# Optimization experiments

Measured on AMD Instinct MI355X. Metric: run time of the kernel, lower is better.

Reference implementation:

```python
import jax, jax.numpy as jnp
import numpy as np

ABS_DIM, HIDDEN, ACTION_DIM, N_TASKS, B = 512, 512, 18, 16, 8192
W_SCALE = 0.001


def setup_inputs() -> dict:
    key = jax.random.key(0)
    k1, k2, k3, k4, k5 = jax.random.split(key, 5)
    x = jax.random.normal(k1, (B, ABS_DIM), dtype=jnp.float32)
    task_id = jax.random.randint(k2, (B,), 0, N_TASKS)
    action = jax.random.randint(k3, (B,), 0, ACTION_DIM)
    # Per-task weight banks (MultiLinear), w_scale=0.001
    W1 = jax.random.normal(k4, (N_TASKS, ABS_DIM, HIDDEN), dtype=jnp.float32) * W_SCALE
    b1 = jnp.zeros((N_TASKS, HIDDEN), dtype=jnp.float32)
    W2 = jax.random.normal(k5, (N_TASKS, HIDDEN, ACTION_DIM), dtype=jnp.float32) * W_SCALE
    b2 = jnp.zeros((N_TASKS, ACTION_DIM), dtype=jnp.float32)
    return {"x": x, "task_id": task_id, "action": action,
            "W1": W1, "b1": b1, "W2": W2, "b2": b2}


def _multi_linear(x, W, b, task_id):
    # x: [B, din], W: [T, din, dout], b: [T, dout]
    # Compute all experts then select per-sample (dense grouped-GEMM form).
    y_all = jnp.einsum('bi,tio->tbo', x, W) + b[:, None, :]  # [T, B, dout]
    rows = jnp.arange(x.shape[0])
    return y_all[task_id, rows]  # [B, dout]


def reference(x, task_id, action, W1, b1, W2, b2):
    h = jax.nn.relu(_multi_linear(x, W1, b1, task_id))          # [B, H]
    logits = _multi_linear(h, W2, b2, task_id)                  # [B, A]
    logprobs = jax.nn.log_softmax(logits, axis=1)               # [B, A]
    rows = jnp.arange(x.shape[0])
    log_pi_a = logprobs[rows, action][:, None]                  # [B, 1]
    ent = -jnp.sum(jnp.exp(logprobs) * logprobs, axis=1, keepdims=True)  # [B, 1]
    # forward output: concat of log_pi_a and entropy (action passes through)
    return jnp.concatenate([log_pi_a, ent], axis=1)             # [B, 2]
```

## Files before the change

kernel.cpp:

```cpp
#include <hip/hip_runtime.h>
#include <hip/hip_bf16.h>

#define B_N   8192
#define DIN   512
#define DH    512
#define NACT  18
#define NTASK 16
#define BM    64
#define BN    64
#define BK    32
#define PJ    20
#define NSLOT 1280
#define SPILL 256

typedef __attribute__((ext_vector_type(8))) short  short8v;
typedef __attribute__((ext_vector_type(8))) unsigned short ushort8v;
typedef __attribute__((ext_vector_type(4))) unsigned short ushort4v;
typedef __attribute__((ext_vector_type(4))) float  float4v;
typedef __attribute__((ext_vector_type(2))) float  float2v;

typedef const __attribute__((address_space(1))) void* gas_ptr;
typedef __attribute__((address_space(3))) void* las_ptr;

__device__ __forceinline__ unsigned short f2bf(float f) {
  union { float f; unsigned int u; } c; c.f = f;
  unsigned int u = c.u;
  u += 0x7fffu + ((u >> 16) & 1u);
  return (unsigned short)(u >> 16);
}

__global__ __launch_bounds__(256) void k_prep(
    const float* __restrict__ W1, const float* __restrict__ W2,
    const int* __restrict__ task_id,
    short* __restrict__ W1T, short* __restrict__ W2T,
    int* __restrict__ tbl, int* __restrict__ rowidx) {
  __shared__ __align__(16) char ldsT[64 * 144];
  __shared__ float ldsB[64 * 19];
  __shared__ int c4[4][NTASK], cur4[4][NTASK];
  int bx = blockIdx.x, tid = threadIdx.x;

  if (bx == 0) {
    if (tid < 64) ((int*)c4)[tid] = 0;
    __syncthreads();
    for (int i = tid; i < B_N; i += 256)
      atomicAdd(&c4[i >> 11][task_id[i]], 1);
    __syncthreads();
    if (tid == 0) {
      int acc = 0;
#pragma unroll
      for (int t = 0; t < NTASK; ++t) {
        int c = c4[0][t] + c4[1][t] + c4[2][t] + c4[3][t];
        tbl[t] = c; tbl[16 + t] = acc;
        int o = acc;
#pragma unroll
        for (int q = 0; q < 4; ++q) { cur4[q][t] = o; o += c4[q][t]; }
        acc += c;
      }
    }
    __syncthreads();
    for (int i = tid; i < B_N; i += 256) {
      int t = task_id[i];
      rowidx[atomicAdd(&cur4[i >> 11][t], 1)] = i;
    }
  } else if (bx <= 1024) {
    int r = bx & 7;
    int q = ((bx - r) >> 3) - (r == 0 ? 1 : 0);
    int t = r + ((q >> 6) << 3);
    int sub = q & 63;
    int kb = sub >> 3, nb = sub & 7;
    int nc4 = tid & 15, kr4 = tid >> 4;
    const float* src = W1 + ((size_t)t * DIN + (size_t)(kb * 64 + kr4 * 4)) * DH
                          + nb * 64 + nc4 * 4;
    float4v r0 = *(const float4v*)(src);
    float4v r1 = *(const float4v*)(src + DH);
    float4v r2 = *(const float4v*)(src + 2 * DH);
    float4v r3 = *(const float4v*)(src + 3 * DH);
#pragma unroll
    for (int i = 0; i < 4; ++i) {
      int n = nc4 * 4 + i;
      ushort4v pk;
      pk[0] = f2bf(r0[i]); pk[1] = f2bf(r1[i]);
      pk[2] = f2bf(r2[i]); pk[3] = f2bf(r3[i]);
      int c = (kr4 >> 1) ^ ((n >> 2) & 7);
      *(ushort4v*)(ldsT + n * 144 + c * 16 + (kr4 & 1) * 8) = pk;
    }
    __syncthreads();
    int n = tid >> 2, k16 = (tid & 3) << 4;
    int c0 = k16 >> 3;
    int f  = (n >> 2) & 7;
    ushort8v v0 = *(ushort8v*)(ldsT + n * 144 + ((c0 ^ f) * 16));
    ushort8v v1 = *(ushort8v*)(ldsT + n * 144 + (((c0 + 1) ^ f) * 16));
    short* dst = W1T + ((size_t)t * DH + nb * 64 + n) * DIN + kb * 64 + k16;
    *(ushort8v*)dst       = v0;
    *(ushort8v*)(dst + 8) = v1;
  } else {
    int u = bx - 1025;
    int t = u >> 3, k0 = (u & 7) * 64;
    for (int i = tid; i < 64 * NACT; i += 256) {
      int kk = i / NACT, j = i - kk * NACT;
      ldsB[kk * 19 + j] = W2[((size_t)t * DIN + k0 + kk) * NACT + j];
    }
    __syncthreads();
    for (int o = tid; o < 32 * 64; o += 256) {
      int j = o >> 6, kk = o & 63;
      float val = (j < NACT) ? ldsB[kk * 19 + j] : 0.0f;
      W2T[((size_t)t * 32 + j) * DIN + k0 + kk] = (short)f2bf(val);
    }
  }
}

__global__ __launch_bounds__(256, 5) void k_gemm1(
    const float* __restrict__ x, const float* __restrict__ bias1,
    const short* __restrict__ W1T, const short* __restrict__ W2Tg,
    const int* __restrict__ tbl, const int* __restrict__ rowidx,
    float* __restrict__ pbuf) {
  __shared__ __align__(16) short sA[2][BM * 40];
  __shared__ __align__(16) short sB[2][BN * BK];
  short* sH  = sA[0];
  short* sW2 = sB[0];
  __shared__ int s_rows[64];
  int tid = threadIdx.x, lane = tid & 63, wave = tid >> 6;

  int b = blockIdx.x;
  int t = -1, rel = 0;
  if (b < NSLOT) {
    int r = b & 7, q = b >> 3;
    int n0t = (tbl[r] + 63) >> 6, n1t = (tbl[r + 8] + 63) >> 6;
    if (q < 8 * n0t) { t = r; rel = q; }
    else if (q < 8 * (n0t + n1t)) { t = r + 8; rel = q - 8 * n0t; }
    else return;
  } else {
    int j = b - NSLOT;
    for (int r = 0; r < 8; ++r) {
      int n0t = (tbl[r] + 63) >> 6, n1t = (tbl[r + 8] + 63) >> 6;
      int P = 8 * (n0t + n1t);
      int S = (P > 160) ? (P - 160) : 0;
      if (j < S) {
        int q = 160 + j;
        if (q < 8 * n0t) { t = r; rel = q; }
        else { t = r + 8; rel = q - 8 * n0t; }
        break;
      }
      j -= S;
    }
    if (t < 0) return;
  }
  int itile = rel >> 3, cs = rel & 7;
  int cnt_t = tbl[t], off_t = tbl[16 + t];
  int row0 = off_t + itile * 64;
  int mcnt = cnt_t - itile * 64; if (mcnt > 64) mcnt = 64;
  int n0 = cs * BN;

  if (tid < 64) {
    int idx = row0 + tid;
    if (idx > B_N - 1) idx = B_N - 1;
    s_rows[tid] = rowidx[idx];
  }
  __syncthreads();

  int arow = tid >> 2, ak8 = (tid & 3) << 3;
  const float* xrow = x + (size_t)s_rows[arow] * DIN + ak8;
  const short* Bbase = W1T + ((size_t)t * DH + n0) * DIN;
  int brow = tid >> 2, bc = tid & 3;
  int bsc = bc ^ ((brow >> 1) & 3);

  float4v La0, La1;
#define LOAD_A(k0e) {                                                        \
    const float* xs_ = xrow + (k0e);                                         \
    La0 = *(const float4v*)xs_;                                              \
    La1 = *(const float4v*)(xs_ + 4); }
#define WRITE_A(buf) {                                                       \
    ushort8v p0;                                                             \
    _Pragma("unroll") for (int i_ = 0; i_ < 4; ++i_) {                       \
      p0[i_] = f2bf(La0[i_]); p0[4 + i_] = f2bf(La1[i_]); }                  \
    *(ushort8v*)&sA[buf][arow * 40 + ak8] = p0; }
#define STAGE_B(buf, k0e)                                                    \
    __builtin_amdgcn_global_load_lds(                                        \
        (gas_ptr)(const void*)(Bbase + (size_t)brow * DIN + (k0e) + bsc * 8),\
        (las_ptr)(void*)(&sB[buf][tid * 8]), 16, 0, 0);

  LOAD_A(0)
  STAGE_B(0, 0)
  WRITE_A(0)
  asm volatile("s_waitcnt vmcnt(0)" ::: "memory");
  __syncthreads();

  float4v acc[4];
#pragma unroll
  for (int i = 0; i < 4; ++i) acc[i] = (float4v)0.0f;

#pragma unroll
  for (int step = 0; step < 16; ++step) {
    const int p = step & 1;
    if (step < 15) {
      LOAD_A((step + 1) * BK)
      STAGE_B(p ^ 1, (step + 1) * BK)
    }
    short8v a, bfr[4];
    {
      int r = wave * 16 + (lane & 15);
      a = *(const short8v*)&sA[p][r * 40 + ((lane >> 4) << 3)];
    }
#pragma unroll
    for (int fn = 0; fn < 4; ++fn) {
      int r = fn * 16 + (lane & 15);
      int c = (lane >> 4) ^ ((r >> 1) & 3);
      bfr[fn] = *(const short8v*)&sB[p][r * BK + c * 8];
    }
#pragma unroll
    for (int fn = 0; fn < 4; ++fn)
      acc[fn] = __builtin_amdgcn_mfma_f32_16x16x32_bf16(a, bfr[fn], acc[fn], 0, 0, 0);
    if (step < 15) {
      WRITE_A(p ^ 1)
    }
    asm volatile("s_waitcnt vmcnt(0)" ::: "memory");
    __syncthreads();
  }

#pragma unroll
  for (int fn = 0; fn < 4; ++fn) {
    int n = fn * 16 + (lane & 15);
    float bias = bias1[t * DH + n0 + n];
#pragma unroll
    for (int r = 0; r < 4; ++r) {
      int m = wave * 16 + ((lane >> 4) << 2) + r;
      float v = fmaxf(acc[fn][r] + bias, 0.0f);
      *(short*)((char*)sH + m * 128 + (((n >> 3) ^ (m & 7)) << 4) + ((n & 7) << 1)) =
          (short)f2bf(v);
    }
  }
  {
    int j = tid >> 3, c2 = tid & 7;
    ushort8v w = *(const ushort8v*)(W2Tg + ((size_t)t * 32 + j) * DIN + n0 + c2 * 8);
    *(ushort8v*)&sW2[(j * 8 + (c2 ^ (j & 7))) * 8] = w;
  }
  __syncthreads();

  float4v acc2[2];
  acc2[0] = (float4v)0.0f; acc2[1] = (float4v)0.0f;
#pragma unroll
  for (int ks = 0; ks < 2; ++ks) {
    int mrow = wave * 16 + (lane & 15);
    int ca = (ks * 4 + (lane >> 4)) ^ (mrow & 7);
    short8v af = *(const short8v*)((char*)sH + mrow * 128 + (ca << 4));
#pragma unroll
    for (int fn = 0; fn < 2; ++fn) {
      int j = fn * 16 + (lane & 15);
      int cb = (ks * 4 + (lane >> 4)) ^ (j & 7);
      short8v bf = *(const short8v*)&sW2[(j * 8 + cb) * 8];
      acc2[fn] = __builtin_amdgcn_mfma_f32_16x16x32_bf16(af, bf, acc2[fn], 0, 0, 0);
    }
  }
#pragma unroll
  for (int fn = 0; fn < 2; ++fn) {
#pragma unroll
    for (int r = 0; r < 4; ++r) {
      int m = wave * 16 + ((lane >> 4) << 2) + r;
      int j = fn * 16 + (lane & 15);
      if (m < mcnt && j < PJ)
        pbuf[((size_t)cs * B_N + row0 + m) * PJ + j] = acc2[fn][r];
    }
  }
#undef STAGE_B
#undef LOAD_A
#undef WRITE_A
}

__global__ __launch_bounds__(256) void k_soft(
    const float* __restrict__ pbuf, const float* __restrict__ bias2,
    const int* __restrict__ task_id, const int* __restrict__ action,
    const int* __restrict__ rowidx, float* __restrict__ out) {
  __shared__ float acc[256 * PJ];
  int tid = threadIdx.x;
  int base = blockIdx.x * 256;
#pragma unroll
  for (int it = 0; it < 5; ++it) {
    int idx = it * 256 + tid;
    int row = idx / 5, j4 = idx - row * 5;
    float4v s = (float4v)0.0f;
#pragma unroll
    for (int c = 0; c < 8; ++c)
      s += *(const float4v*)&pbuf[((size_t)c * B_N + base + row) * PJ + j4 * 4];
    *(float4v*)&acc[row * PJ + j4 * 4] = s;
  }
  __syncthreads();

  int srow = base + tid;
  int orig = rowidx[srow];
  int t = task_id[orig], act = action[orig];
  float lg[NACT];
#pragma unroll
  for (int j = 0; j < NACT; ++j) lg[j] = acc[tid * PJ + j] + bias2[t * NACT + j];
  float mx = lg[0];
#pragma unroll
  for (int j = 1; j < NACT; ++j) mx = fmaxf(mx, lg[j]);
  float s1 = 0.0f, s2 = 0.0f, la = 0.0f;
#pragma unroll
  for (int j = 0; j < NACT; ++j) {
    float e = __expf(lg[j] - mx);
    s1 += e; s2 += e * lg[j];
    la = (j == act) ? lg[j] : la;
  }
  float logZ = __logf(s1);
  float2v o;
  o[0] = la - mx - logZ;
  o[1] = (mx + logZ) - s2 / s1;
  *(float2v*)(out + (size_t)orig * 2) = o;
}

extern "C" void kernel_launch(void* const* d_in, const int* in_sizes, int n_in,
                              void* d_out, int out_size, void* d_ws, size_t ws_size,
                              hipStream_t stream) {
  const float* x       = (const float*)d_in[0];
  const int*   task_id = (const int*)d_in[1];
  const int*   action  = (const int*)d_in[2];
  const float* W1      = (const float*)d_in[3];
  const float* b1      = (const float*)d_in[4];
  const float* W2      = (const float*)d_in[5];
  const float* b2      = (const float*)d_in[6];
  float* out = (float*)d_out;

  char* ws = (char*)d_ws;
  int* tbl    = (int*)ws;
  int* rowidx = (int*)(ws + 4096);
  size_t off = 36864;
  short* W1T  = (short*)(ws + off);  off += (size_t)NTASK * DH * DIN * 2;
  short* W2T  = (short*)(ws + off);  off += (size_t)NTASK * 32 * DIN * 2;
  float* pbuf = (float*)(ws + off);

  k_prep<<<1153, 256, 0, stream>>>(W1, W2, task_id, W1T, W2T, tbl, rowidx);
  k_gemm1<<<NSLOT + SPILL, 256, 0, stream>>>(x, b1, W1T, W2T, tbl, rowidx, pbuf);
  k_soft<<<32, 256, 0, stream>>>(pbuf, b2, task_id, action, rowidx, out);
}
```

Baseline: 43.54 us.

## Drop W1 bf16 pre-transpose pass; convert W1 fp32 tiles inside GEMM

Removes the prep-kernel stage that converted and transposed all of W1 to a bf16 workspace copy. The GEMM now loads fp32 W1 directly, converts it to bf16 in registers and writes a transposed, padded LDS tile, replacing the async global_load_lds staging. This drops a full read and write of the weight bank and most of the prep launch. In exchange each GEMM block reads twice the weight bytes in fp32, repeated across row tiles of the same task, and the B loads go through registers instead of the async LDS path.

```diff
diff --git a/kernel.cpp b/kernel.cpp
--- a/kernel.cpp
+++ b/kernel.cpp
@@ -29,12 +29,9 @@
   return (unsigned short)(u >> 16);
 }
 
-__global__ __launch_bounds__(256) void k_prep(
-    const float* __restrict__ W1, const float* __restrict__ W2,
-    const int* __restrict__ task_id,
-    short* __restrict__ W1T, short* __restrict__ W2T,
-    int* __restrict__ tbl, int* __restrict__ rowidx) {
-  __shared__ __align__(16) char ldsT[64 * 144];
+__global__ __launch_bounds__(256) void k_pre(
+    const float* __restrict__ W2, const int* __restrict__ task_id,
+    short* __restrict__ W2T, int* __restrict__ tbl, int* __restrict__ rowidx) {
   __shared__ float ldsB[64 * 19];
   __shared__ int c4[4][NTASK], cur4[4][NTASK];
   int bx = blockIdx.x, tid = threadIdx.x;
@@ -62,39 +59,8 @@
       int t = task_id[i];
       rowidx[atomicAdd(&cur4[i >> 11][t], 1)] = i;
     }
-  } else if (bx <= 1024) {
-    int r = bx & 7;
-    int q = ((bx - r) >> 3) - (r == 0 ? 1 : 0);
-    int t = r + ((q >> 6) << 3);
-    int sub = q & 63;
-    int kb = sub >> 3, nb = sub & 7;
-    int nc4 = tid & 15, kr4 = tid >> 4;
-    const float* src = W1 + ((size_t)t * DIN + (size_t)(kb * 64 + kr4 * 4)) * DH
-                          + nb * 64 + nc4 * 4;
-    float4v r0 = *(const float4v*)(src);
-    float4v r1 = *(const float4v*)(src + DH);
-    float4v r2 = *(const float4v*)(src + 2 * DH);
-    float4v r3 = *(const float4v*)(src + 3 * DH);
-#pragma unroll
-    for (int i = 0; i < 4; ++i) {
-      int n = nc4 * 4 + i;
-      ushort4v pk;
-      pk[0] = f2bf(r0[i]); pk[1] = f2bf(r1[i]);
-      pk[2] = f2bf(r2[i]); pk[3] = f2bf(r3[i]);
-      int c = (kr4 >> 1) ^ ((n >> 2) & 7);
-      *(ushort4v*)(ldsT + n * 144 + c * 16 + (kr4 & 1) * 8) = pk;
-    }
-    __syncthreads();
-    int n = tid >> 2, k16 = (tid & 3) << 4;
-    int c0 = k16 >> 3;
-    int f  = (n >> 2) & 7;
-    ushort8v v0 = *(ushort8v*)(ldsT + n * 144 + ((c0 ^ f) * 16));
-    ushort8v v1 = *(ushort8v*)(ldsT + n * 144 + (((c0 + 1) ^ f) * 16));
-    short* dst = W1T + ((size_t)t * DH + nb * 64 + n) * DIN + kb * 64 + k16;
-    *(ushort8v*)dst       = v0;
-    *(ushort8v*)(dst + 8) = v1;
   } else {
-    int u = bx - 1025;
+    int u = bx - 1;
     int t = u >> 3, k0 = (u & 7) * 64;
     for (int i = tid; i < 64 * NACT; i += 256) {
       int kk = i / NACT, j = i - kk * NACT;
@@ -111,11 +77,11 @@
 
 __global__ __launch_bounds__(256, 5) void k_gemm1(
     const float* __restrict__ x, const float* __restrict__ bias1,
-    const short* __restrict__ W1T, const short* __restrict__ W2Tg,
+    const float* __restrict__ W1, const short* __restrict__ W2Tg,
     const int* __restrict__ tbl, const int* __restrict__ rowidx,
     float* __restrict__ pbuf) {
   __shared__ __align__(16) short sA[2][BM * 40];
-  __shared__ __align__(16) short sB[2][BN * BK];
+  __shared__ __align__(16) short sB[2][BN * 40];
   short* sH  = sA[0];
   short* sW2 = sB[0];
   __shared__ int s_rows[64];
@@ -160,11 +126,12 @@
 
   int arow = tid >> 2, ak8 = (tid & 3) << 3;
   const float* xrow = x + (size_t)s_rows[arow] * DIN + ak8;
-  const short* Bbase = W1T + ((size_t)t * DH + n0) * DIN;
-  int brow = tid >> 2, bc = tid & 3;
-  int bsc = bc ^ ((brow >> 1) & 3);
+  int bh = tid >> 7, bkq = (tid >> 4) & 7, bnq = tid & 15;
+  int bn = bnq * 4 + bh * 2;
+  const float* w1b = W1 + ((size_t)t * DIN + bkq * 4) * DH + n0 + bn;
 
   float4v La0, La1;
+  float2v Lb0, Lb1, Lb2, Lb3;
 #define LOAD_A(k0e) {                                                        \
     const float* xs_ = xrow + (k0e);                                         \
     La0 = *(const float4v*)xs_;                                              \
@@ -174,15 +141,23 @@
     _Pragma("unroll") for (int i_ = 0; i_ < 4; ++i_) {                       \
       p0[i_] = f2bf(La0[i_]); p0[4 + i_] = f2bf(La1[i_]); }                  \
     *(ushort8v*)&sA[buf][arow * 40 + ak8] = p0; }
-#define STAGE_B(buf, k0e)                                                    \
-    __builtin_amdgcn_global_load_lds(                                        \
-        (gas_ptr)(const void*)(Bbase + (size_t)brow * DIN + (k0e) + bsc * 8),\
-        (las_ptr)(void*)(&sB[buf][tid * 8]), 16, 0, 0);
+#define LOAD_B(k0e) {                                                        \
+    const float* wb_ = w1b + (size_t)(k0e) * DH;                             \
+    Lb0 = *(const float2v*)(wb_);                                            \
+    Lb1 = *(const float2v*)(wb_ + DH);                                       \
+    Lb2 = *(const float2v*)(wb_ + 2 * DH);                                   \
+    Lb3 = *(const float2v*)(wb_ + 3 * DH); }
+#define WRITE_B(buf) {                                                       \
+    _Pragma("unroll") for (int c_ = 0; c_ < 2; ++c_) {                       \
+      ushort4v pk;                                                           \
+      pk[0] = f2bf(Lb0[c_]); pk[1] = f2bf(Lb1[c_]);                          \
+      pk[2] = f2bf(Lb2[c_]); pk[3] = f2bf(Lb3[c_]);                          \
+      *(ushort4v*)&sB[buf][(bn + c_) * 40 + bkq * 4] = pk; } }
 
   LOAD_A(0)
-  STAGE_B(0, 0)
+  LOAD_B(0)
   WRITE_A(0)
-  asm volatile("s_waitcnt vmcnt(0)" ::: "memory");
+  WRITE_B(0)
   __syncthreads();
 
   float4v acc[4];
@@ -194,7 +169,7 @@
     const int p = step & 1;
     if (step < 15) {
       LOAD_A((step + 1) * BK)
-      STAGE_B(p ^ 1, (step + 1) * BK)
+      LOAD_B((step + 1) * BK)
     }
     short8v a, bfr[4];
     {
@@ -204,16 +179,15 @@
 #pragma unroll
     for (int fn = 0; fn < 4; ++fn) {
       int r = fn * 16 + (lane & 15);
-      int c = (lane >> 4) ^ ((r >> 1) & 3);
-      bfr[fn] = *(const short8v*)&sB[p][r * BK + c * 8];
+      bfr[fn] = *(const short8v*)&sB[p][r * 40 + ((lane >> 4) << 3)];
     }
 #pragma unroll
     for (int fn = 0; fn < 4; ++fn)
       acc[fn] = __builtin_amdgcn_mfma_f32_16x16x32_bf16(a, bfr[fn], acc[fn], 0, 0, 0);
     if (step < 15) {
       WRITE_A(p ^ 1)
-    }
-    asm volatile("s_waitcnt vmcnt(0)" ::: "memory");
+      WRITE_B(p ^ 1)
+    }
     __syncthreads();
   }
 
@@ -261,9 +235,10 @@
         pbuf[((size_t)cs * B_N + row0 + m) * PJ + j] = acc2[fn][r];
     }
   }
-#undef STAGE_B
 #undef LOAD_A
 #undef WRITE_A
+#undef LOAD_B
+#undef WRITE_B
 }
 
 __global__ __launch_bounds__(256) void k_soft(
@@ -324,11 +299,10 @@
   int* tbl    = (int*)ws;
   int* rowidx = (int*)(ws + 4096);
   size_t off = 36864;
-  short* W1T  = (short*)(ws + off);  off += (size_t)NTASK * DH * DIN * 2;
   short* W2T  = (short*)(ws + off);  off += (size_t)NTASK * 32 * DIN * 2;
   float* pbuf = (float*)(ws + off);
 
-  k_prep<<<1153, 256, 0, stream>>>(W1, W2, task_id, W1T, W2T, tbl, rowidx);
-  k_gemm1<<<NSLOT + SPILL, 256, 0, stream>>>(x, b1, W1T, W2T, tbl, rowidx, pbuf);
+  k_pre<<<129, 256, 0, stream>>>(W2, task_id, W2T, tbl, rowidx);
+  k_gemm1<<<NSLOT + SPILL, 256, 0, stream>>>(x, b1, W1, W2T, tbl, rowidx, pbuf);
   k_soft<<<32, 256, 0, stream>>>(pbuf, b2, task_id, action, rowidx, out);
 }
```

Result: slower. 48.60 us (+11.6%).
